# Optimization experiments

Measured on AMD Instinct MI355X. Metric: run time of the kernel, lower is better.

## Reference

```python
import jax, jax.numpy as jnp
import numpy as np

B, S, D, H = 2, 2048, 1024, 16
DK = D // H


def setup_inputs() -> dict:
    key = jax.random.key(0)
    ks = jax.random.split(key, 8)
    w_scale = 1.0 / np.sqrt(D)
    return {
        "query": jax.random.normal(ks[0], (B, S, D), jnp.float32),
        "key": jax.random.normal(ks[1], (B, S, D), jnp.float32),
        "value": jax.random.normal(ks[2], (B, S, D), jnp.float32),
        "Wq": jax.random.normal(ks[3], (D, D), jnp.float32) * w_scale,
        "bq": jnp.zeros((D,), jnp.float32),
        "Wk": jax.random.normal(ks[4], (D, D), jnp.float32) * w_scale,
        "bk": jnp.zeros((D,), jnp.float32),
        "Wv": jax.random.normal(ks[5], (D, D), jnp.float32) * w_scale,
        "bv": jnp.zeros((D,), jnp.float32),
        "Wo": jax.random.normal(ks[6], (D, D), jnp.float32) * w_scale,
        "bo": jnp.zeros((D,), jnp.float32),
    }


def _heads(x, W, b):
    # torch nn.Linear: y = x @ W.T + b ; then [B,S,D] -> [B,H,S,DK]
    y = x @ W.T + b
    return y.reshape(x.shape[0], x.shape[1], H, DK).transpose(0, 2, 1, 3)


def reference(query, key, value, Wq, bq, Wk, bk, Wv, bv, Wo, bo):
    q = _heads(query, Wq, bq)   # [B,H,S,DK]
    k = _heads(key, Wk, bk)
    v = _heads(value, Wv, bv)
    scale = 100.0 / np.sqrt(DK).astype(np.float32)
    scores = jnp.einsum("bhqd,bhkd->bhqk", q, k) * scale  # [B,H,Sq,Sk]
    prob = jax.nn.softmax(scores, axis=-1)                 # dropout p=0 -> identity
    out = jnp.einsum("bhqk,bhkd->bhqd", prob, v)           # [B,H,Sq,DK]
    mean_atp = prob.mean(axis=(1, 2))                      # mean over heads & query -> [B,Sk]
    out = out.transpose(0, 2, 1, 3).reshape(query.shape[0], -1, D)
    out = out @ Wo.T + bo
    return out, mean_atp
```

## Files before the change

### kernel.cpp

```cpp
#include <hip/hip_runtime.h>
#include <hip/hip_bf16.h>


#define B_  2
#define S_  2048
#define D_  1024
#define H_  16
#define DK_ 64

typedef __bf16 bf16x8 __attribute__((ext_vector_type(8)));
typedef float f32x4  __attribute__((ext_vector_type(4)));

__global__ __launch_bounds__(256)
void split3_kernel(const float* __restrict__ x, __bf16* __restrict__ y,
                   int n, int mode)
{
  int i = (blockIdx.x * 256 + threadIdx.x) * 8;
  if (i >= n) return;
  float4 a = *(const float4*)(x + i);
  float4 b = *(const float4*)(x + i + 4);
  float xs[8] = {a.x, a.y, a.z, a.w, b.x, b.y, b.z, b.w};
  __bf16 out[24];
#pragma unroll
  for (int j = 0; j < 8; j++) {
    float v = xs[j];
    __bf16 hi = (__bf16)v;
    __bf16 lo = (__bf16)(v - (float)hi);
    if (mode == 0) { out[3*j] = hi; out[3*j+1] = hi; out[3*j+2] = lo; }
    else           { out[3*j] = hi; out[3*j+1] = lo; out[3*j+2] = hi; }
  }
  *(bf16x8*)(y + 3 * (size_t)i)      = *(bf16x8*)&out[0];
  *(bf16x8*)(y + 3 * (size_t)i + 8)  = *(bf16x8*)&out[8];
  *(bf16x8*)(y + 3 * (size_t)i + 16) = *(bf16x8*)&out[16];
}

__global__ __launch_bounds__(256)
void tobf16_kernel(const float* __restrict__ x, __bf16* __restrict__ y, int n)
{
  int i = (blockIdx.x * 256 + threadIdx.x) * 8;
  if (i >= n) return;
  float4 a = *(const float4*)(x + i);
  float4 b = *(const float4*)(x + i + 4);
  __bf16 out[8] = {(__bf16)a.x, (__bf16)a.y, (__bf16)a.z, (__bf16)a.w,
                   (__bf16)b.x, (__bf16)b.y, (__bf16)b.z, (__bf16)b.w};
  *(bf16x8*)(y + i) = *(bf16x8*)&out[0];
}

#define TM 128
#define TN 128
#define TK 64
#define KSTR 72

__global__ __launch_bounds__(256)
void gemm_mfma(const __bf16* __restrict__ X, const __bf16* __restrict__ W,
               const float* __restrict__ bias, void* __restrict__ Y,
               void* __restrict__ Y2, int M, int N, int K, int out_mode)
{
  __shared__ __bf16 Xa[TM * KSTR];
  __shared__ __bf16 Wb[TN * KSTR];

  const int tid  = threadIdx.x;
  const int lane = tid & 63;
  const int w    = tid >> 6;
  const int c    = lane & 15;
  const int quad = lane >> 4;
  const int row0 = blockIdx.y * TM;
  const int col0 = blockIdx.x * TN;
  const int wr   = (w >> 1) * 64;
  const int wc   = (w & 1) * 64;

  f32x4 acc[4][4];
#pragma unroll
  for (int i = 0; i < 4; i++)
#pragma unroll
    for (int j = 0; j < 4; j++) acc[i][j] = (f32x4){0.f, 0.f, 0.f, 0.f};

  for (int k0 = 0; k0 < K; k0 += TK) {
    __syncthreads();
#pragma unroll
    for (int i = 0; i < 4; i++) {
      int idx = i * 256 + tid;
      int r = idx >> 3, kc = idx & 7;
      *(bf16x8*)&Xa[r * KSTR + kc * 8] =
          *(const bf16x8*)(X + (size_t)(row0 + r) * K + k0 + kc * 8);
      *(bf16x8*)&Wb[r * KSTR + kc * 8] =
          *(const bf16x8*)(W + (size_t)(col0 + r) * K + k0 + kc * 8);
    }
    __syncthreads();

#pragma unroll
    for (int cc = 0; cc < 2; cc++) {
      bf16x8 af[4], bf[4];
#pragma unroll
      for (int i = 0; i < 4; i++)
        af[i] = *(const bf16x8*)&Xa[(wr + i * 16 + c) * KSTR + cc * 32 + quad * 8];
#pragma unroll
      for (int j = 0; j < 4; j++)
        bf[j] = *(const bf16x8*)&Wb[(wc + j * 16 + c) * KSTR + cc * 32 + quad * 8];
#pragma unroll
      for (int i = 0; i < 4; i++)
#pragma unroll
        for (int j = 0; j < 4; j++)
          acc[i][j] = __builtin_amdgcn_mfma_f32_16x16x32_bf16(af[i], bf[j],
                                                              acc[i][j], 0, 0, 0);
    }
  }

#pragma unroll
  for (int i = 0; i < 4; i++) {
#pragma unroll
    for (int j = 0; j < 4; j++) {
      int col = col0 + wc + j * 16 + c;
      float bcol = bias[col];
#pragma unroll
      for (int r = 0; r < 4; r++) {
        int row = row0 + wr + i * 16 + quad * 4 + r;
        float v = acc[i][j][r] + bcol;
        if (out_mode == 0) {
          ((float*)Y)[(size_t)row * N + col] = v;
        } else {
          int b2 = row >> 11, s = row & (S_ - 1);
          int h = col >> 6, dk = col & 63;
          if (out_mode == 1) {
            size_t off = ((size_t)(b2 * H_ + h) * S_ + s) * DK_ + dk;
            __bf16 hi = (__bf16)v;
            ((__bf16*)Y)[off]  = hi;
            ((__bf16*)Y2)[off] = (__bf16)(v - (float)hi);
          } else {
            ((__bf16*)Y)[((size_t)(b2 * H_ + h) * DK_ + dk) * S_ + s] = (__bf16)v;
          }
        }
      }
    }
  }
}

#define LSTR 72

__global__ __launch_bounds__(256)
void attn_mfma(const __bf16* __restrict__ qh_ws, const __bf16* __restrict__ ql_ws,
               const __bf16* __restrict__ kh_ws, const __bf16* __restrict__ kl_ws,
               const __bf16* __restrict__ vt_ws, __bf16* __restrict__ attn_out,
               float* __restrict__ atp_out)
{
  __shared__ __bf16 Kh[64 * LSTR];
  __shared__ __bf16 Kl[64 * LSTR];
  __shared__ __bf16 Vt[64 * LSTR];
  __shared__ __bf16 Ps[4][16 * LSTR];
  __shared__ float  atp_lds[S_];

  const int tid  = threadIdx.x;
  const int lane = tid & 63;
  const int w    = tid >> 6;
  const int c    = lane & 15;
  const int quad = lane >> 4;
  const int qb   = blockIdx.x;
  const int h    = blockIdx.y;
  const int b    = blockIdx.z;

  const size_t bh = (size_t)(b * H_ + h);
  const __bf16* qhg = qh_ws + (bh * S_ + qb * 64) * DK_;
  const __bf16* qlg = ql_ws + (bh * S_ + qb * 64) * DK_;
  const __bf16* khg = kh_ws + bh * S_ * DK_;
  const __bf16* klg = kl_ws + bh * S_ * DK_;
  const __bf16* vg  = vt_ws + bh * DK_ * S_;

  bf16x8 qhf[2], qlf[2];
  {
    const __bf16* qrow = qhg + (size_t)(w * 16 + c) * DK_;
    qhf[0] = *(const bf16x8*)(qrow + quad * 8);
    qhf[1] = *(const bf16x8*)(qrow + 32 + quad * 8);
    const __bf16* qrow2 = qlg + (size_t)(w * 16 + c) * DK_;
    qlf[0] = *(const bf16x8*)(qrow2 + quad * 8);
    qlf[1] = *(const bf16x8*)(qrow2 + 32 + quad * 8);
  }

  const float scale = 12.5f;
  float m_r[4], l_r[4];
#pragma unroll
  for (int r = 0; r < 4; r++) { m_r[r] = -1e30f; l_r[r] = 0.f; }

  for (int kt = 0; kt < S_ / 64; kt++) {
    __syncthreads();
#pragma unroll
    for (int i = 0; i < 2; i++) {
      int idx = i * 256 + tid;
      int key = idx >> 3, dch = idx & 7;
      *(bf16x8*)&Kh[key * LSTR + dch * 8] =
          *(const bf16x8*)(khg + (size_t)(kt * 64 + key) * DK_ + dch * 8);
      *(bf16x8*)&Kl[key * LSTR + dch * 8] =
          *(const bf16x8*)(klg + (size_t)(kt * 64 + key) * DK_ + dch * 8);
    }
    __syncthreads();

    f32x4 sc[4];
#pragma unroll
    for (int nt = 0; nt < 4; nt++) {
      f32x4 acc = {0.f, 0.f, 0.f, 0.f};
#pragma unroll
      for (int cc = 0; cc < 2; cc++) {
        bf16x8 bh8 = *(const bf16x8*)&Kh[(nt * 16 + c) * LSTR + cc * 32 + quad * 8];
        bf16x8 bl8 = *(const bf16x8*)&Kl[(nt * 16 + c) * LSTR + cc * 32 + quad * 8];
        acc = __builtin_amdgcn_mfma_f32_16x16x32_bf16(qhf[cc], bh8, acc, 0, 0, 0);
        acc = __builtin_amdgcn_mfma_f32_16x16x32_bf16(qhf[cc], bl8, acc, 0, 0, 0);
        acc = __builtin_amdgcn_mfma_f32_16x16x32_bf16(qlf[cc], bh8, acc, 0, 0, 0);
      }
      sc[nt] = acc;
    }

    float tm[4];
#pragma unroll
    for (int r = 0; r < 4; r++) {
      tm[r] = fmaxf(fmaxf(sc[0][r], sc[1][r]), fmaxf(sc[2][r], sc[3][r]));
      tm[r] *= scale;
    }
#pragma unroll
    for (int o = 1; o < 16; o <<= 1)
#pragma unroll
      for (int r = 0; r < 4; r++) tm[r] = fmaxf(tm[r], __shfl_xor(tm[r], o, 64));

    float psum[4];
#pragma unroll
    for (int r = 0; r < 4; r++) {
      float mnew = fmaxf(m_r[r], tm[r]);
      float p = 0.f;
#pragma unroll
      for (int nt = 0; nt < 4; nt++) p += __expf(sc[nt][r] * scale - mnew);
      psum[r] = p;
      l_r[r] *= __expf(m_r[r] - mnew);
      m_r[r] = mnew;
    }
#pragma unroll
    for (int o = 1; o < 16; o <<= 1)
#pragma unroll
      for (int r = 0; r < 4; r++) psum[r] += __shfl_xor(psum[r], o, 64);
#pragma unroll
    for (int r = 0; r < 4; r++) l_r[r] += psum[r];
  }

  float rl[4];
#pragma unroll
  for (int r = 0; r < 4; r++) rl[r] = 1.0f / l_r[r];

  for (int i = tid; i < S_; i += 256) atp_lds[i] = 0.f;

  f32x4 of[4];
#pragma unroll
  for (int nt = 0; nt < 4; nt++) of[nt] = (f32x4){0.f, 0.f, 0.f, 0.f};

  __bf16* ps = Ps[w];

  for (int kt = 0; kt < S_ / 64; kt++) {
    __syncthreads();
#pragma unroll
    for (int i = 0; i < 2; i++) {
      int idx = i * 256 + tid;
      int key = idx >> 3, dch = idx & 7;
      *(bf16x8*)&Kh[key * LSTR + dch * 8] =
          *(const bf16x8*)(khg + (size_t)(kt * 64 + key) * DK_ + dch * 8);
      *(bf16x8*)&Kl[key * LSTR + dch * 8] =
          *(const bf16x8*)(klg + (size_t)(kt * 64 + key) * DK_ + dch * 8);
      *(bf16x8*)&Vt[key * LSTR + dch * 8] =
          *(const bf16x8*)(vg + (size_t)key * S_ + kt * 64 + dch * 8);
    }
    __syncthreads();

#pragma unroll
    for (int nt = 0; nt < 4; nt++) {
      f32x4 acc = {0.f, 0.f, 0.f, 0.f};
#pragma unroll
      for (int cc = 0; cc < 2; cc++) {
        bf16x8 bh8 = *(const bf16x8*)&Kh[(nt * 16 + c) * LSTR + cc * 32 + quad * 8];
        bf16x8 bl8 = *(const bf16x8*)&Kl[(nt * 16 + c) * LSTR + cc * 32 + quad * 8];
        acc = __builtin_amdgcn_mfma_f32_16x16x32_bf16(qhf[cc], bh8, acc, 0, 0, 0);
        acc = __builtin_amdgcn_mfma_f32_16x16x32_bf16(qhf[cc], bl8, acc, 0, 0, 0);
        acc = __builtin_amdgcn_mfma_f32_16x16x32_bf16(qlf[cc], bh8, acc, 0, 0, 0);
      }
      float t = 0.f;
#pragma unroll
      for (int r = 0; r < 4; r++) {
        float p = __expf(acc[r] * scale - m_r[r]) * rl[r];
        ps[(quad * 4 + r) * LSTR + nt * 16 + c] = (__bf16)p;
        t += p;
      }
      t += __shfl_xor(t, 16, 64);
      t += __shfl_xor(t, 32, 64);
      if (quad == 0) atomicAdd(&atp_lds[kt * 64 + nt * 16 + c], t);
    }

#pragma unroll
    for (int nt = 0; nt < 4; nt++) {
#pragma unroll
      for (int cc = 0; cc < 2; cc++) {
        bf16x8 pa = *(const bf16x8*)&ps[c * LSTR + cc * 32 + quad * 8];
        bf16x8 vb = *(const bf16x8*)&Vt[(nt * 16 + c) * LSTR + cc * 32 + quad * 8];
        of[nt] = __builtin_amdgcn_mfma_f32_16x16x32_bf16(pa, vb, of[nt], 0, 0, 0);
      }
    }
  }

#pragma unroll
  for (int nt = 0; nt < 4; nt++)
#pragma unroll
    for (int r = 0; r < 4; r++)
      attn_out[((size_t)(b * S_ + qb * 64 + w * 16 + quad * 4 + r)) * D_
               + h * DK_ + nt * 16 + c] = (__bf16)of[nt][r];

  __syncthreads();
  const float inv = 1.0f / ((float)H_ * (float)S_);
  for (int i = tid; i < S_; i += 256)
    atomicAdd(&atp_out[b * S_ + i], atp_lds[i] * inv);
}

__global__ void zero_f32(float* __restrict__ p, int n) {
  int i = blockIdx.x * 256 + threadIdx.x;
  if (i < n) p[i] = 0.f;
}

extern "C" void kernel_launch(void* const* d_in, const int* in_sizes, int n_in,
                              void* d_out, int out_size, void* d_ws, size_t ws_size,
                              hipStream_t stream)
{
  const float* query = (const float*)d_in[0];
  const float* key_  = (const float*)d_in[1];
  const float* value = (const float*)d_in[2];
  const float* Wq = (const float*)d_in[3];
  const float* bq = (const float*)d_in[4];
  const float* Wk = (const float*)d_in[5];
  const float* bk = (const float*)d_in[6];
  const float* Wv = (const float*)d_in[7];
  const float* bv = (const float*)d_in[8];
  const float* Wo = (const float*)d_in[9];
  const float* bo = (const float*)d_in[10];

  float* out = (float*)d_out;
  float* atp = out + (size_t)B_ * S_ * D_;

  const size_t NE = (size_t)B_ * S_ * D_;
  const size_t NW = (size_t)D_ * D_;
  __bf16* p = (__bf16*)d_ws;
  __bf16* qcat3 = p;               p += 3 * NE;
  __bf16* kcat3 = p;               p += 3 * NE;
  __bf16* wqc3  = p;               p += 3 * NW;
  __bf16* wkc3  = p;               p += 3 * NW;
  __bf16* vxb   = p;               p += NE;
  __bf16* wvb   = p;               p += NW;
  __bf16* wob   = p;               p += NW;
  __bf16* qh_ws = p;               p += NE;
  __bf16* ql_ws = p;               p += NE;
  __bf16* kh_ws = p;               p += NE;
  __bf16* kl_ws = p;               p += NE;
  __bf16* vt_ws = kcat3;
  __bf16* a_ws  = qcat3;

  const int M = B_ * S_;

  split3_kernel<<<NE / (256 * 8), 256, 0, stream>>>(query, qcat3, (int)NE, 0);
  split3_kernel<<<NE / (256 * 8), 256, 0, stream>>>(key_,  kcat3, (int)NE, 0);
  split3_kernel<<<NW / (256 * 8), 256, 0, stream>>>(Wq, wqc3, (int)NW, 1);
  split3_kernel<<<NW / (256 * 8), 256, 0, stream>>>(Wk, wkc3, (int)NW, 1);
  tobf16_kernel<<<NE / (256 * 8), 256, 0, stream>>>(value, vxb, (int)NE);
  tobf16_kernel<<<NW / (256 * 8), 256, 0, stream>>>(Wv, wvb, (int)NW);
  tobf16_kernel<<<NW / (256 * 8), 256, 0, stream>>>(Wo, wob, (int)NW);

  dim3 ggrid(D_ / TN, M / TM);
  gemm_mfma<<<ggrid, 256, 0, stream>>>(qcat3, wqc3, bq, qh_ws, ql_ws, M, D_, 3 * D_, 1);
  gemm_mfma<<<ggrid, 256, 0, stream>>>(kcat3, wkc3, bk, kh_ws, kl_ws, M, D_, 3 * D_, 1);
  gemm_mfma<<<ggrid, 256, 0, stream>>>(vxb,   wvb,  bv, vt_ws, nullptr, M, D_, D_, 2);

  zero_f32<<<(B_ * S_ + 255) / 256, 256, 0, stream>>>(atp, B_ * S_);

  attn_mfma<<<dim3(S_ / 64, H_, B_), 256, 0, stream>>>(qh_ws, ql_ws, kh_ws, kl_ws,
                                                       vt_ws, a_ws, atp);

  gemm_mfma<<<ggrid, 256, 0, stream>>>(a_ws, wob, bo, out, nullptr, M, D_, D_, 0);
}
```

Before: 585.9 us.

## Double attention query rows per wave and use direct global-to-LDS loads in GEMM

Each wave in the attention kernel now handles 32 query rows instead of 16, so every K/V tile staged in LDS is reused by twice as many MFMAs and the grid is halved. The P tile is now kept in LDS as fp32 with a padded stride and converted to bf16 when it is read back for the PV MFMA. The GEMM stages its tiles with global_load_lds 16-byte direct loads into unpadded LDS instead of going through registers. Risks are higher register pressure, fewer attention blocks to fill the CUs, and LDS bank conflicts from the unpadded GEMM layout.

```diff
diff --git a/kernel.cpp b/kernel.cpp
--- a/kernel.cpp
+++ b/kernel.cpp
@@ -10,6 +10,12 @@
 
 typedef __bf16 bf16x8 __attribute__((ext_vector_type(8)));
 typedef float f32x4  __attribute__((ext_vector_type(4)));
+
+__device__ __forceinline__ void ld_g2l16(const __bf16* g, __bf16* l) {
+  __builtin_amdgcn_global_load_lds(
+      (const __attribute__((address_space(1))) void*)g,
+      (__attribute__((address_space(3))) void*)l, 16, 0, 0);
+}
 
 __global__ __launch_bounds__(256)
 void split3_kernel(const float* __restrict__ x, __bf16* __restrict__ y,
@@ -49,15 +55,14 @@
 #define TM 128
 #define TN 128
 #define TK 64
-#define KSTR 72
 
 __global__ __launch_bounds__(256)
 void gemm_mfma(const __bf16* __restrict__ X, const __bf16* __restrict__ W,
                const float* __restrict__ bias, void* __restrict__ Y,
                void* __restrict__ Y2, int M, int N, int K, int out_mode)
 {
-  __shared__ __bf16 Xa[TM * KSTR];
-  __shared__ __bf16 Wb[TN * KSTR];
+  __shared__ __align__(16) __bf16 Xa[TM * TK];
+  __shared__ __align__(16) __bf16 Wb[TN * TK];
 
   const int tid  = threadIdx.x;
   const int lane = tid & 63;
@@ -79,12 +84,10 @@
     __syncthreads();
 #pragma unroll
     for (int i = 0; i < 4; i++) {
-      int idx = i * 256 + tid;
-      int r = idx >> 3, kc = idx & 7;
-      *(bf16x8*)&Xa[r * KSTR + kc * 8] =
-          *(const bf16x8*)(X + (size_t)(row0 + r) * K + k0 + kc * 8);
-      *(bf16x8*)&Wb[r * KSTR + kc * 8] =
-          *(const bf16x8*)(W + (size_t)(col0 + r) * K + k0 + kc * 8);
+      int chunk = w * 256 + i * 64 + lane;
+      int r = chunk >> 3, dch = chunk & 7;
+      ld_g2l16(X + (size_t)(row0 + r) * K + k0 + dch * 8, &Xa[chunk * 8]);
+      ld_g2l16(W + (size_t)(col0 + r) * K + k0 + dch * 8, &Wb[chunk * 8]);
     }
     __syncthreads();
 
@@ -93,10 +96,10 @@
       bf16x8 af[4], bf[4];
 #pragma unroll
       for (int i = 0; i < 4; i++)
-        af[i] = *(const bf16x8*)&Xa[(wr + i * 16 + c) * KSTR + cc * 32 + quad * 8];
+        af[i] = *(const bf16x8*)&Xa[(wr + i * 16 + c) * TK + cc * 32 + quad * 8];
 #pragma unroll
       for (int j = 0; j < 4; j++)
-        bf[j] = *(const bf16x8*)&Wb[(wc + j * 16 + c) * KSTR + cc * 32 + quad * 8];
+        bf[j] = *(const bf16x8*)&Wb[(wc + j * 16 + c) * TK + cc * 32 + quad * 8];
 #pragma unroll
       for (int i = 0; i < 4; i++)
 #pragma unroll
@@ -136,6 +139,34 @@
 }
 
 #define LSTR 72
+#define PSTR 68
+
+__device__ __forceinline__ void qk_scores(const __bf16* __restrict__ Kh,
+                                          const __bf16* __restrict__ Kl,
+                                          const bf16x8 qhf[2][2],
+                                          const bf16x8 qlf[2][2],
+                                          int c, int quad, f32x4 sc[2][4])
+{
+#pragma unroll
+  for (int nt = 0; nt < 4; nt++) {
+#pragma unroll
+    for (int rg = 0; rg < 2; rg++) sc[rg][nt] = (f32x4){0.f, 0.f, 0.f, 0.f};
+#pragma unroll
+    for (int cc = 0; cc < 2; cc++) {
+      bf16x8 bh8 = *(const bf16x8*)&Kh[(nt * 16 + c) * LSTR + cc * 32 + quad * 8];
+      bf16x8 bl8 = *(const bf16x8*)&Kl[(nt * 16 + c) * LSTR + cc * 32 + quad * 8];
+#pragma unroll
+      for (int rg = 0; rg < 2; rg++) {
+        sc[rg][nt] = __builtin_amdgcn_mfma_f32_16x16x32_bf16(qhf[rg][cc], bh8,
+                                                             sc[rg][nt], 0, 0, 0);
+        sc[rg][nt] = __builtin_amdgcn_mfma_f32_16x16x32_bf16(qhf[rg][cc], bl8,
+                                                             sc[rg][nt], 0, 0, 0);
+        sc[rg][nt] = __builtin_amdgcn_mfma_f32_16x16x32_bf16(qlf[rg][cc], bh8,
+                                                             sc[rg][nt], 0, 0, 0);
+      }
+    }
+  }
+}
 
 __global__ __launch_bounds__(256)
 void attn_mfma(const __bf16* __restrict__ qh_ws, const __bf16* __restrict__ ql_ws,
@@ -143,10 +174,10 @@
                const __bf16* __restrict__ vt_ws, __bf16* __restrict__ attn_out,
                float* __restrict__ atp_out)
 {
-  __shared__ __bf16 Kh[64 * LSTR];
-  __shared__ __bf16 Kl[64 * LSTR];
-  __shared__ __bf16 Vt[64 * LSTR];
-  __shared__ __bf16 Ps[4][16 * LSTR];
+  __shared__ __align__(16) __bf16 Kh[64 * LSTR];
+  __shared__ __align__(16) __bf16 Kl[64 * LSTR];
+  __shared__ __align__(16) __bf16 Vt[64 * LSTR];
+  __shared__ __align__(16) float  Ps[4][32 * PSTR];
   __shared__ float  atp_lds[S_];
 
   const int tid  = threadIdx.x;
@@ -159,26 +190,29 @@
   const int b    = blockIdx.z;
 
   const size_t bh = (size_t)(b * H_ + h);
-  const __bf16* qhg = qh_ws + (bh * S_ + qb * 64) * DK_;
-  const __bf16* qlg = ql_ws + (bh * S_ + qb * 64) * DK_;
+  const __bf16* qhg = qh_ws + (bh * S_ + qb * 128) * DK_;
+  const __bf16* qlg = ql_ws + (bh * S_ + qb * 128) * DK_;
   const __bf16* khg = kh_ws + bh * S_ * DK_;
   const __bf16* klg = kl_ws + bh * S_ * DK_;
   const __bf16* vg  = vt_ws + bh * DK_ * S_;
 
-  bf16x8 qhf[2], qlf[2];
-  {
-    const __bf16* qrow = qhg + (size_t)(w * 16 + c) * DK_;
-    qhf[0] = *(const bf16x8*)(qrow + quad * 8);
-    qhf[1] = *(const bf16x8*)(qrow + 32 + quad * 8);
-    const __bf16* qrow2 = qlg + (size_t)(w * 16 + c) * DK_;
-    qlf[0] = *(const bf16x8*)(qrow2 + quad * 8);
-    qlf[1] = *(const bf16x8*)(qrow2 + 32 + quad * 8);
+  bf16x8 qhf[2][2], qlf[2][2];
+#pragma unroll
+  for (int rg = 0; rg < 2; rg++) {
+    const __bf16* qrow = qhg + (size_t)(w * 32 + rg * 16 + c) * DK_;
+    qhf[rg][0] = *(const bf16x8*)(qrow + quad * 8);
+    qhf[rg][1] = *(const bf16x8*)(qrow + 32 + quad * 8);
+    const __bf16* qrow2 = qlg + (size_t)(w * 32 + rg * 16 + c) * DK_;
+    qlf[rg][0] = *(const bf16x8*)(qrow2 + quad * 8);
+    qlf[rg][1] = *(const bf16x8*)(qrow2 + 32 + quad * 8);
   }
 
   const float scale = 12.5f;
-  float m_r[4], l_r[4];
-#pragma unroll
-  for (int r = 0; r < 4; r++) { m_r[r] = -1e30f; l_r[r] = 0.f; }
+  float m_r[2][4], l_r[2][4];
+#pragma unroll
+  for (int rg = 0; rg < 2; rg++)
+#pragma unroll
+    for (int r = 0; r < 4; r++) { m_r[rg][r] = -1e30f; l_r[rg][r] = 0.f; }
 
   for (int kt = 0; kt < S_ / 64; kt++) {
     __syncthreads();
@@ -193,62 +227,65 @@
     }
     __syncthreads();
 
-    f32x4 sc[4];
-#pragma unroll
-    for (int nt = 0; nt < 4; nt++) {
-      f32x4 acc = {0.f, 0.f, 0.f, 0.f};
-#pragma unroll
-      for (int cc = 0; cc < 2; cc++) {
-        bf16x8 bh8 = *(const bf16x8*)&Kh[(nt * 16 + c) * LSTR + cc * 32 + quad * 8];
-        bf16x8 bl8 = *(const bf16x8*)&Kl[(nt * 16 + c) * LSTR + cc * 32 + quad * 8];
-        acc = __builtin_amdgcn_mfma_f32_16x16x32_bf16(qhf[cc], bh8, acc, 0, 0, 0);
-        acc = __builtin_amdgcn_mfma_f32_16x16x32_bf16(qhf[cc], bl8, acc, 0, 0, 0);
-        acc = __builtin_amdgcn_mfma_f32_16x16x32_bf16(qlf[cc], bh8, acc, 0, 0, 0);
+    f32x4 sc[2][4];
+    qk_scores(Kh, Kl, qhf, qlf, c, quad, sc);
+
+    float tm[2][4], psum[2][4];
+#pragma unroll
+    for (int rg = 0; rg < 2; rg++)
+#pragma unroll
+      for (int r = 0; r < 4; r++) {
+        tm[rg][r] = fmaxf(fmaxf(sc[rg][0][r], sc[rg][1][r]),
+                          fmaxf(sc[rg][2][r], sc[rg][3][r])) * scale;
       }
-      sc[nt] = acc;
-    }
-
-    float tm[4];
-#pragma unroll
-    for (int r = 0; r < 4; r++) {
-      tm[r] = fmaxf(fmaxf(sc[0][r], sc[1][r]), fmaxf(sc[2][r], sc[3][r]));
-      tm[r] *= scale;
-    }
 #pragma unroll
     for (int o = 1; o < 16; o <<= 1)
 #pragma unroll
-      for (int r = 0; r < 4; r++) tm[r] = fmaxf(tm[r], __shfl_xor(tm[r], o, 64));
-
-    float psum[4];
-#pragma unroll
-    for (int r = 0; r < 4; r++) {
-      float mnew = fmaxf(m_r[r], tm[r]);
-      float p = 0.f;
-#pragma unroll
-      for (int nt = 0; nt < 4; nt++) p += __expf(sc[nt][r] * scale - mnew);
-      psum[r] = p;
-      l_r[r] *= __expf(m_r[r] - mnew);
-      m_r[r] = mnew;
-    }
+      for (int rg = 0; rg < 2; rg++)
+#pragma unroll
+        for (int r = 0; r < 4; r++)
+          tm[rg][r] = fmaxf(tm[rg][r], __shfl_xor(tm[rg][r], o, 64));
+
+#pragma unroll
+    for (int rg = 0; rg < 2; rg++)
+#pragma unroll
+      for (int r = 0; r < 4; r++) {
+        float mnew = fmaxf(m_r[rg][r], tm[rg][r]);
+        float p = 0.f;
+#pragma unroll
+        for (int nt = 0; nt < 4; nt++) p += __expf(sc[rg][nt][r] * scale - mnew);
+        psum[rg][r] = p;
+        l_r[rg][r] *= __expf(m_r[rg][r] - mnew);
+        m_r[rg][r] = mnew;
+      }
 #pragma unroll
     for (int o = 1; o < 16; o <<= 1)
 #pragma unroll
-      for (int r = 0; r < 4; r++) psum[r] += __shfl_xor(psum[r], o, 64);
-#pragma unroll
-    for (int r = 0; r < 4; r++) l_r[r] += psum[r];
-  }
-
-  float rl[4];
-#pragma unroll
-  for (int r = 0; r < 4; r++) rl[r] = 1.0f / l_r[r];
+      for (int rg = 0; rg < 2; rg++)
+#pragma unroll
+        for (int r = 0; r < 4; r++)
+          psum[rg][r] += __shfl_xor(psum[rg][r], o, 64);
+#pragma unroll
+    for (int rg = 0; rg < 2; rg++)
+#pragma unroll
+      for (int r = 0; r < 4; r++) l_r[rg][r] += psum[rg][r];
+  }
+
+  float rl[2][4];
+#pragma unroll
+  for (int rg = 0; rg < 2; rg++)
+#pragma unroll
+    for (int r = 0; r < 4; r++) rl[rg][r] = 1.0f / l_r[rg][r];
 
   for (int i = tid; i < S_; i += 256) atp_lds[i] = 0.f;
 
-  f32x4 of[4];
-#pragma unroll
-  for (int nt = 0; nt < 4; nt++) of[nt] = (f32x4){0.f, 0.f, 0.f, 0.f};
-
-  __bf16* ps = Ps[w];
+  f32x4 of[2][4];
+#pragma unroll
+  for (int rg = 0; rg < 2; rg++)
+#pragma unroll
+    for (int nt = 0; nt < 4; nt++) of[rg][nt] = (f32x4){0.f, 0.f, 0.f, 0.f};
+
+  float* ps = Ps[w];
 
   for (int kt = 0; kt < S_ / 64; kt++) {
     __syncthreads();
@@ -265,46 +302,57 @@
     }
     __syncthreads();
 
+    f32x4 sc[2][4];
+    qk_scores(Kh, Kl, qhf, qlf, c, quad, sc);
+
 #pragma unroll
     for (int nt = 0; nt < 4; nt++) {
-      f32x4 acc = {0.f, 0.f, 0.f, 0.f};
-#pragma unroll
-      for (int cc = 0; cc < 2; cc++) {
-        bf16x8 bh8 = *(const bf16x8*)&Kh[(nt * 16 + c) * LSTR + cc * 32 + quad * 8];
-        bf16x8 bl8 = *(const bf16x8*)&Kl[(nt * 16 + c) * LSTR + cc * 32 + quad * 8];
-        acc = __builtin_amdgcn_mfma_f32_16x16x32_bf16(qhf[cc], bh8, acc, 0, 0, 0);
-        acc = __builtin_amdgcn_mfma_f32_16x16x32_bf16(qhf[cc], bl8, acc, 0, 0, 0);
-        acc = __builtin_amdgcn_mfma_f32_16x16x32_bf16(qlf[cc], bh8, acc, 0, 0, 0);
-      }
       float t = 0.f;
 #pragma unroll
-      for (int r = 0; r < 4; r++) {
-        float p = __expf(acc[r] * scale - m_r[r]) * rl[r];
-        ps[(quad * 4 + r) * LSTR + nt * 16 + c] = (__bf16)p;
-        t += p;
-      }
+      for (int rg = 0; rg < 2; rg++)
+#pragma unroll
+        for (int r = 0; r < 4; r++) {
+          float p = __expf(sc[rg][nt][r] * scale - m_r[rg][r]) * rl[rg][r];
+          ps[(rg * 16 + quad * 4 + r) * PSTR + nt * 16 + c] = p;
+          t += p;
+        }
       t += __shfl_xor(t, 16, 64);
       t += __shfl_xor(t, 32, 64);
       if (quad == 0) atomicAdd(&atp_lds[kt * 64 + nt * 16 + c], t);
     }
 
 #pragma unroll
-    for (int nt = 0; nt < 4; nt++) {
+    for (int rg = 0; rg < 2; rg++) {
+      bf16x8 pa[2];
 #pragma unroll
       for (int cc = 0; cc < 2; cc++) {
-        bf16x8 pa = *(const bf16x8*)&ps[c * LSTR + cc * 32 + quad * 8];
-        bf16x8 vb = *(const bf16x8*)&Vt[(nt * 16 + c) * LSTR + cc * 32 + quad * 8];
-        of[nt] = __builtin_amdgcn_mfma_f32_16x16x32_bf16(pa, vb, of[nt], 0, 0, 0);
+        const float* pp = &ps[(rg * 16 + c) * PSTR + cc * 32 + quad * 8];
+        f32x4 p0 = *(const f32x4*)pp;
+        f32x4 p1 = *(const f32x4*)(pp + 4);
+        bf16x8 v8;
+#pragma unroll
+        for (int j = 0; j < 4; j++) { v8[j] = (__bf16)p0[j]; v8[4 + j] = (__bf16)p1[j]; }
+        pa[cc] = v8;
       }
-    }
-  }
-
-#pragma unroll
-  for (int nt = 0; nt < 4; nt++)
-#pragma unroll
-    for (int r = 0; r < 4; r++)
-      attn_out[((size_t)(b * S_ + qb * 64 + w * 16 + quad * 4 + r)) * D_
-               + h * DK_ + nt * 16 + c] = (__bf16)of[nt][r];
+#pragma unroll
+      for (int nt = 0; nt < 4; nt++)
+#pragma unroll
+        for (int cc = 0; cc < 2; cc++) {
+          bf16x8 vb = *(const bf16x8*)&Vt[(nt * 16 + c) * LSTR + cc * 32 + quad * 8];
+          of[rg][nt] = __builtin_amdgcn_mfma_f32_16x16x32_bf16(pa[cc], vb,
+                                                               of[rg][nt], 0, 0, 0);
+        }
+    }
+  }
+
+#pragma unroll
+  for (int rg = 0; rg < 2; rg++)
+#pragma unroll
+    for (int nt = 0; nt < 4; nt++)
+#pragma unroll
+      for (int r = 0; r < 4; r++)
+        attn_out[((size_t)(b * S_ + qb * 128 + w * 32 + rg * 16 + quad * 4 + r)) * D_
+                 + h * DK_ + nt * 16 + c] = (__bf16)of[rg][nt][r];
 
   __syncthreads();
   const float inv = 1.0f / ((float)H_ * (float)S_);
@@ -370,8 +418,8 @@
 
   zero_f32<<<(B_ * S_ + 255) / 256, 256, 0, stream>>>(atp, B_ * S_);
 
-  attn_mfma<<<dim3(S_ / 64, H_, B_), 256, 0, stream>>>(qh_ws, ql_ws, kh_ws, kl_ws,
-                                                       vt_ws, a_ws, atp);
+  attn_mfma<<<dim3(S_ / 128, H_, B_), 256, 0, stream>>>(qh_ws, ql_ws, kh_ws, kl_ws,
+                                                        vt_ws, a_ws, atp);
 
   gemm_mfma<<<ggrid, 256, 0, stream>>>(a_ws, wob, bo, out, nullptr, M, D_, D_, 0);
 }
```

New measurement: 543.4 us. 7.3% less time.
